# Kernel tuning notes

Hardware: AMD Instinct MI355X
Metric: run time of the kernel (lower is better)

The kernel has to match this reference:

```python
import jax, jax.numpy as jnp
import numpy as np

ALPHA = 0.2  # LeakyReLU negative slope (init arg `alpha`)
N, F_IN, F_OUT = 8192, 512, 256


def setup_inputs() -> dict:
    key = jax.random.key(0)
    k1, k2, k3, k4 = jax.random.split(key, 4)
    x = jax.random.normal(k1, (N, F_IN), dtype=jnp.float32)
    adj = jax.random.randint(k2, (N, N), 0, 2, dtype=jnp.int32)
    W = jax.random.normal(k3, (F_IN, F_OUT), dtype=jnp.float32) * (1.0 / np.sqrt(F_IN))
    a = jax.random.normal(k4, (2 * F_OUT, 1), dtype=jnp.float32) * (1.0 / np.sqrt(F_IN))
    return {"x": x, "adj": adj, "W": W, "a": a}


def reference(x, adj, W, a):
    h = x @ W  # [N, F_OUT]
    f_out = W.shape[1]
    # e[i,j] = LeakyReLU(a1 . h_i + a2 . h_j); computed without the O(N^2*2F) concat
    f1 = h @ a[:f_out, 0]   # [N]
    f2 = h @ a[f_out:, 0]   # [N]
    s = f1[:, None] + f2[None, :]  # [N, N]
    e = jnp.where(s >= 0, s, ALPHA * s)
    # Faithful to the source bug: -9e15 * zeros_like == zeros, so masked entries are 0.0
    att = jnp.where(adj > 0, e, jnp.zeros((), dtype=e.dtype))
    att = jax.nn.softmax(att, axis=1)
    # dropout is identity in eval mode
    h_prime = att @ h  # [N, F_OUT]
    return jax.nn.elu(h_prime)  # concat=True branch
```

## Files before the change

kernel.cpp:

```cpp
#include <hip/hip_runtime.h>
#include <stdint.h>

#define NN 8192
#define FIN 512
#define FOUT 256
#define ALPHA 0.2f
#define KSPLIT 4
#define JT 64
#define NT ((NN / KSPLIT) / JT)

typedef float f32x4 __attribute__((ext_vector_type(4)));
typedef short s16x8 __attribute__((ext_vector_type(8)));

__device__ __forceinline__ uint16_t f2bf(float f) {
  union { float f; uint32_t u; } v; v.f = f;
  uint32_t u = v.u + 0x7fffu + ((v.u >> 16) & 1u);
  return (uint16_t)(u >> 16);
}

__global__ __launch_bounds__(256) void k_wa(const float* __restrict__ W,
                                            const float* __restrict__ a,
                                            float* __restrict__ wa1, float* __restrict__ wa2) {
  __shared__ float a1[256], a2[256];
  int tid = threadIdx.x;
  a1[tid] = a[tid];
  a2[tid] = a[tid + 256];
  __syncthreads();
  int m = blockIdx.x * 256 + tid;
  const float* wrow = W + (size_t)m * FOUT;
  float s1 = 0.f, s2 = 0.f;
  for (int k = 0; k < FOUT; k += 4) {
    f32x4 v = *(const f32x4*)(wrow + k);
#pragma unroll
    for (int i = 0; i < 4; i++) {
      s1 += v[i] * a1[k + i];
      s2 += v[i] * a2[k + i];
    }
  }
  wa1[m] = s1; wa2[m] = s2;
}

__global__ __launch_bounds__(256) void k_f1f2(const float* __restrict__ x,
                                              const float* __restrict__ wa1,
                                              const float* __restrict__ wa2,
                                              float* __restrict__ f1, float* __restrict__ f2,
                                              uint16_t* __restrict__ xb,
                                              float* __restrict__ l_arr) {
  __shared__ float s1[512], s2[512];
  int tid = threadIdx.x;
  if (tid < 4) l_arr[blockIdx.x * 4 + tid] = 0.f;
  s1[tid] = wa1[tid]; s1[tid + 256] = wa1[tid + 256];
  s2[tid] = wa2[tid]; s2[tid + 256] = wa2[tid + 256];
  __syncthreads();
  int w = tid >> 6, l = tid & 63;
  int row = blockIdx.x * 4 + w;
  const float* xr = x + (size_t)row * FIN + l * 8;
  f32x4 v0 = *(const f32x4*)xr;
  f32x4 v1 = *(const f32x4*)(xr + 4);
  uint4 pk;
  pk.x = (uint32_t)f2bf(v0[0]) | ((uint32_t)f2bf(v0[1]) << 16);
  pk.y = (uint32_t)f2bf(v0[2]) | ((uint32_t)f2bf(v0[3]) << 16);
  pk.z = (uint32_t)f2bf(v1[0]) | ((uint32_t)f2bf(v1[1]) << 16);
  pk.w = (uint32_t)f2bf(v1[2]) | ((uint32_t)f2bf(v1[3]) << 16);
  *(uint4*)(xb + (size_t)row * FIN + l * 8) = pk;
  int kb = l * 8;
  float d1 = 0.f, d2 = 0.f;
#pragma unroll
  for (int i = 0; i < 4; i++) {
    d1 += v0[i] * s1[kb + i] + v1[i] * s1[kb + 4 + i];
    d2 += v0[i] * s2[kb + i] + v1[i] * s2[kb + 4 + i];
  }
#pragma unroll
  for (int off = 32; off; off >>= 1) {
    d1 += __shfl_down(d1, off);
    d2 += __shfl_down(d2, off);
  }
  if (l == 0) { f1[row] = d1; f2[row] = d2; }
}

__global__ __launch_bounds__(256) void k_prep_wt(const float* __restrict__ W,
                                                 uint16_t* __restrict__ wt) {
  int idx = blockIdx.x * 256 + threadIdx.x;
  int f  = idx >> 7;
  int k4 = (idx & 127) * 4;
  ushort4 o;
  o.x = f2bf(W[(size_t)(k4 + 0) * FOUT + f]);
  o.y = f2bf(W[(size_t)(k4 + 1) * FOUT + f]);
  o.z = f2bf(W[(size_t)(k4 + 2) * FOUT + f]);
  o.w = f2bf(W[(size_t)(k4 + 3) * FOUT + f]);
  *(ushort4*)(wt + (size_t)f * FIN + k4) = o;
}

__global__ __launch_bounds__(256, 2) void k_gemm_h(const uint16_t* __restrict__ xb,
                                                   const uint16_t* __restrict__ wt,
                                                   uint16_t* __restrict__ h) {
  __shared__ uint16_t Xs[64][40];
  __shared__ uint16_t Ws[64][40];
  int i0 = blockIdx.x * 64;
  int f0 = blockIdx.y * 64;
  int tid = threadIdx.x;
  int w = tid >> 6, l = tid & 63;
  int q = l >> 4, r16 = l & 15;
  f32x4 acc[4];
#pragma unroll
  for (int b = 0; b < 4; b++) acc[b] = (f32x4)0.f;

  int srow = tid >> 2, sch = tid & 3;
  for (int k0 = 0; k0 < FIN; k0 += 32) {
    uint4 xv = *(const uint4*)(xb + (size_t)(i0 + srow) * FIN + k0 + sch * 8);
    uint4 wv = *(const uint4*)(wt + (size_t)(f0 + srow) * FIN + k0 + sch * 8);
    *(uint4*)(&Xs[srow][sch * 8]) = xv;
    *(uint4*)(&Ws[srow][sch * 8]) = wv;
    __syncthreads();
    s16x8 A = *(const s16x8*)(&Xs[w * 16 + r16][q * 8]);
    s16x8 B[4];
#pragma unroll
    for (int b = 0; b < 4; b++) B[b] = *(const s16x8*)(&Ws[b * 16 + r16][q * 8]);
#pragma unroll
    for (int b = 0; b < 4; b++)
      acc[b] = __builtin_amdgcn_mfma_f32_16x16x32_bf16(A, B[b], acc[b], 0, 0, 0);
    __syncthreads();
  }
#pragma unroll
  for (int b = 0; b < 4; b++)
#pragma unroll
    for (int reg = 0; reg < 4; reg++) {
      int row = i0 + w * 16 + q * 4 + reg;
      int col = f0 + b * 16 + r16;
      h[(size_t)row * FOUT + col] = f2bf(acc[b][reg]);
    }
}

__global__ __launch_bounds__(256) void k_transpose(const uint16_t* __restrict__ h,
                                                   uint16_t* __restrict__ ht) {
  __shared__ uint16_t T[64][72];
  int i0 = blockIdx.x * 64, f0 = blockIdx.y * 64;
  int tid = threadIdx.x;
#pragma unroll
  for (int p = 0; p < 2; p++) {
    int idx = tid + p * 256;
    int r = idx >> 3, c8 = idx & 7;
    uint4 v = *(const uint4*)(h + (size_t)(i0 + r) * FOUT + f0 + c8 * 8);
    *(uint4*)(&T[r][c8 * 8]) = v;
  }
  __syncthreads();
#pragma unroll
  for (int p = 0; p < 2; p++) {
    int idx = tid + p * 256;
    int fr = idx >> 3, ic8 = idx & 7;
    s16x8 v;
#pragma unroll
    for (int j = 0; j < 8; j++) v[j] = (short)T[ic8 * 8 + j][fr];
    *(s16x8*)(ht + (size_t)(f0 + fr) * NN + i0 + ic8 * 8) = v;
  }
}

__global__ __launch_bounds__(256, 2) void k_att(const int* __restrict__ adj,
                                                const uint16_t* __restrict__ ht,
                                                const float* __restrict__ f1,
                                                const float* __restrict__ f2,
                                                float* __restrict__ l_arr,
                                                float* __restrict__ part) {
  __shared__ uint16_t Ps[2][64][72];
  __shared__ uint16_t Hs[256][72];
  __shared__ float Fs[NN / KSPLIT];
  int i0 = blockIdx.x * 64;
  int jbase = blockIdx.y * (NN / KSPLIT);
  int tid = threadIdx.x;
  int w = tid >> 6, l = tid & 63;
  int q = l >> 4, r16 = l & 15;
  int prow = tid >> 2, pch = tid & 3;
  int hr8 = l >> 3, hc8 = l & 7;
  float f1i = f1[i0 + prow];
  float lsum = 0.f;

  {
    f32x4 a0 = *(const f32x4*)(f2 + jbase + tid * 8);
    f32x4 a1 = *(const f32x4*)(f2 + jbase + tid * 8 + 4);
    *(f32x4*)(&Fs[tid * 8]) = a0;
    *(f32x4*)(&Fs[tid * 8 + 4]) = a1;
  }
  __syncthreads();

  f32x4 acc[4][4];
#pragma unroll
  for (int a = 0; a < 4; a++)
#pragma unroll
    for (int b = 0; b < 4; b++) acc[a][b] = (f32x4)0.f;

  const int* arow = adj + (size_t)(i0 + prow) * NN + jbase + pch * 16;
  const uint16_t* hrow = ht + (size_t)(w * 64 + hr8) * NN + jbase + hc8 * 8;

  int4 adv[4];
  uint4 hv[8];
#pragma unroll
  for (int t = 0; t < 4; ++t) adv[t] = *(const int4*)(arow + t * 4);
#pragma unroll
  for (int p = 0; p < 8; ++p) hv[p] = *(const uint4*)(hrow + (size_t)p * 8 * NN);

  for (int s = 0; s < NT; ++s) {
    int jl = s * JT;
    f32x4 F0 = *(const f32x4*)(&Fs[jl + pch * 16]);
    f32x4 F1 = *(const f32x4*)(&Fs[jl + pch * 16 + 4]);
    f32x4 F2 = *(const f32x4*)(&Fs[jl + pch * 16 + 8]);
    f32x4 F3 = *(const f32x4*)(&Fs[jl + pch * 16 + 12]);
    s16x8 pv0, pv1;
#define PC(dst, kk, Ac, Fc) { float s_ = f1i + (Fc); float e_ = s_ > 0.f ? s_ : ALPHA * s_; \
      float p_ = ((Ac) != 0) ? __expf(e_) : 1.0f; lsum += p_; dst[kk] = (short)f2bf(p_); }
    PC(pv0, 0, adv[0].x, F0[0]) PC(pv0, 1, adv[0].y, F0[1])
    PC(pv0, 2, adv[0].z, F0[2]) PC(pv0, 3, adv[0].w, F0[3])
    PC(pv0, 4, adv[1].x, F1[0]) PC(pv0, 5, adv[1].y, F1[1])
    PC(pv0, 6, adv[1].z, F1[2]) PC(pv0, 7, adv[1].w, F1[3])
    PC(pv1, 0, adv[2].x, F2[0]) PC(pv1, 1, adv[2].y, F2[1])
    PC(pv1, 2, adv[2].z, F2[2]) PC(pv1, 3, adv[2].w, F2[3])
    PC(pv1, 4, adv[3].x, F3[0]) PC(pv1, 5, adv[3].y, F3[1])
    PC(pv1, 6, adv[3].z, F3[2]) PC(pv1, 7, adv[3].w, F3[3])
#undef PC
    uint16_t (*Pc)[72] = Ps[s & 1];
    *(s16x8*)(&Pc[prow][pch * 16]) = pv0;
    *(s16x8*)(&Pc[prow][pch * 16 + 8]) = pv1;
#pragma unroll
    for (int p = 0; p < 8; ++p)
      *(uint4*)(&Hs[w * 64 + p * 8 + hr8][hc8 * 8]) = hv[p];
    if (s + 1 < NT) {
      int jn = jl + JT;
#pragma unroll
      for (int t = 0; t < 4; ++t) adv[t] = *(const int4*)(arow + jn + t * 4);
#pragma unroll
      for (int p = 0; p < 8; ++p) hv[p] = *(const uint4*)(hrow + (size_t)p * 8 * NN + jn);
    }
    asm volatile("s_waitcnt lgkmcnt(0)" ::: "memory");
    __builtin_amdgcn_s_barrier();
    asm volatile("" ::: "memory");
#pragma unroll
    for (int c = 0; c < 2; ++c) {
      s16x8 Af[4], Bf[4];
#pragma unroll
      for (int a = 0; a < 4; ++a) Af[a] = *(const s16x8*)(&Pc[a * 16 + r16][c * 32 + q * 8]);
#pragma unroll
      for (int b = 0; b < 4; ++b) Bf[b] = *(const s16x8*)(&Hs[w * 64 + b * 16 + r16][c * 32 + q * 8]);
#pragma unroll
      for (int a = 0; a < 4; ++a)
#pragma unroll
        for (int b = 0; b < 4; ++b)
          acc[a][b] = __builtin_amdgcn_mfma_f32_16x16x32_bf16(Af[a], Bf[b], acc[a][b], 0, 0, 0);
    }
  }

  lsum += __shfl_down(lsum, 2);
  lsum += __shfl_down(lsum, 1);
  if (pch == 0) atomicAdd(&l_arr[i0 + prow], lsum);

  float* pb = part + (size_t)blockIdx.y * ((size_t)NN * FOUT);
#pragma unroll
  for (int a = 0; a < 4; a++)
#pragma unroll
    for (int b = 0; b < 4; b++)
#pragma unroll
      for (int reg = 0; reg < 4; reg++) {
        int row = i0 + a * 16 + q * 4 + reg;
        int col = w * 64 + b * 16 + r16;
        pb[(size_t)row * FOUT + col] = acc[a][b][reg];
      }
}

__global__ __launch_bounds__(256) void k_combine(const float* __restrict__ part,
                                                 const float* __restrict__ l_arr,
                                                 float* __restrict__ out) {
  int idx = (blockIdx.x * 256 + threadIdx.x) * 4;
  float r = 1.0f / l_arr[idx >> 8];
  f32x4 sum = (f32x4)0.f;
#pragma unroll
  for (int p = 0; p < KSPLIT; p++)
    sum += *(const f32x4*)(part + (size_t)p * (NN * FOUT) + idx);
  f32x4 o;
#pragma unroll
  for (int i = 0; i < 4; i++) {
    float v = sum[i] * r;
    o[i] = v > 0.f ? v : (__expf(v) - 1.f);
  }
  *(f32x4*)(out + idx) = o;
}

extern "C" void kernel_launch(void* const* d_in, const int* in_sizes, int n_in,
                              void* d_out, int out_size, void* d_ws, size_t ws_size,
                              hipStream_t stream) {
  const float* x   = (const float*)d_in[0];
  const int*   adj = (const int*)d_in[1];
  const float* W   = (const float*)d_in[2];
  const float* a   = (const float*)d_in[3];
  float* out = (float*)d_out;

  char* ws = (char*)d_ws;
  float*    wa1   = (float*)ws;
  float*    wa2   = wa1 + 512;
  float*    f1    = wa2 + 512;
  float*    f2    = f1 + NN;
  float*    l_arr = f2 + NN;
  uint16_t* wt    = (uint16_t*)(l_arr + NN);
  uint16_t* xb    = wt + (size_t)FOUT * FIN;
  uint16_t* h     = xb + (size_t)NN * FIN;
  uint16_t* ht    = h + (size_t)NN * FOUT;
  float*    part  = (float*)(ht + (size_t)NN * FOUT);

  k_wa<<<2, 256, 0, stream>>>(W, a, wa1, wa2);
  k_f1f2<<<NN / 4, 256, 0, stream>>>(x, wa1, wa2, f1, f2, xb, l_arr);
  k_prep_wt<<<128, 256, 0, stream>>>(W, wt);
  k_gemm_h<<<dim3(NN / 64, FOUT / 64), 256, 0, stream>>>(xb, wt, h);
  k_transpose<<<dim3(NN / 64, FOUT / 64), 256, 0, stream>>>(h, ht);
  k_att<<<dim3(NN / 64, KSPLIT), 256, 0, stream>>>(adj, ht, f1, f2, l_arr, part);
  k_combine<<<NN * FOUT / 1024, 256, 0, stream>>>(part, l_arr, out);
}
```

Baseline: 539.4 us.

## Shrink attention tile to 32x32 and raise occupancy in k_att

Restructures the fused attention kernel to use 32-row by 32-column tiles instead of 64x64. It drops the shared-memory f2 staging in favour of direct global loads, shrinks LDS and register use, and raises launch bounds to 4 blocks per CU with twice as many blocks in the grid. The aim is more parallelism and occupancy for the memory-bound adjacency stream. The cost is that the ht tile is reloaded from L2 twice as often per output row and each barrier now covers only one MFMA k-step.

```diff
diff --git a/kernel.cpp b/kernel.cpp
--- a/kernel.cpp
+++ b/kernel.cpp
@@ -6,7 +6,8 @@
 #define FOUT 256
 #define ALPHA 0.2f
 #define KSPLIT 4
-#define JT 64
+#define JT 32
+#define IT 32
 #define NT ((NN / KSPLIT) / JT)
 
 typedef float f32x4 __attribute__((ext_vector_type(4)));
@@ -155,105 +156,87 @@
   }
 }
 
-__global__ __launch_bounds__(256, 2) void k_att(const int* __restrict__ adj,
+__global__ __launch_bounds__(256, 4) void k_att(const int* __restrict__ adj,
                                                 const uint16_t* __restrict__ ht,
                                                 const float* __restrict__ f1,
                                                 const float* __restrict__ f2,
                                                 float* __restrict__ l_arr,
                                                 float* __restrict__ part) {
-  __shared__ uint16_t Ps[2][64][72];
-  __shared__ uint16_t Hs[256][72];
-  __shared__ float Fs[NN / KSPLIT];
-  int i0 = blockIdx.x * 64;
+  __shared__ uint16_t Ps[2][32][40];
+  __shared__ uint16_t Hs[256][40];
+  int i0 = blockIdx.x * IT;
   int jbase = blockIdx.y * (NN / KSPLIT);
   int tid = threadIdx.x;
   int w = tid >> 6, l = tid & 63;
   int q = l >> 4, r16 = l & 15;
-  int prow = tid >> 2, pch = tid & 3;
-  int hr8 = l >> 3, hc8 = l & 7;
+  int prow = tid >> 3, pch = tid & 7;
+  int hr = l >> 2, hc = l & 3;
   float f1i = f1[i0 + prow];
   float lsum = 0.f;
 
-  {
-    f32x4 a0 = *(const f32x4*)(f2 + jbase + tid * 8);
-    f32x4 a1 = *(const f32x4*)(f2 + jbase + tid * 8 + 4);
-    *(f32x4*)(&Fs[tid * 8]) = a0;
-    *(f32x4*)(&Fs[tid * 8 + 4]) = a1;
-  }
-  __syncthreads();
-
-  f32x4 acc[4][4];
-#pragma unroll
-  for (int a = 0; a < 4; a++)
+  const int*      arow = adj + (size_t)(i0 + prow) * NN + jbase + pch * 4;
+  const float*    frow = f2 + jbase + pch * 4;
+  const uint16_t* hrow = ht + (size_t)(w * 64 + hr) * NN + jbase + hc * 8;
+
+  f32x4 acc[2][4];
+#pragma unroll
+  for (int a = 0; a < 2; a++)
 #pragma unroll
     for (int b = 0; b < 4; b++) acc[a][b] = (f32x4)0.f;
 
-  const int* arow = adj + (size_t)(i0 + prow) * NN + jbase + pch * 16;
-  const uint16_t* hrow = ht + (size_t)(w * 64 + hr8) * NN + jbase + hc8 * 8;
-
-  int4 adv[4];
-  uint4 hv[8];
-#pragma unroll
-  for (int t = 0; t < 4; ++t) adv[t] = *(const int4*)(arow + t * 4);
-#pragma unroll
-  for (int p = 0; p < 8; ++p) hv[p] = *(const uint4*)(hrow + (size_t)p * 8 * NN);
+  int4 adv = *(const int4*)(arow);
+  f32x4 F  = *(const f32x4*)(frow);
+  uint4 hv[4];
+#pragma unroll
+  for (int p = 0; p < 4; ++p) hv[p] = *(const uint4*)(hrow + (size_t)p * 16 * NN);
 
   for (int s = 0; s < NT; ++s) {
-    int jl = s * JT;
-    f32x4 F0 = *(const f32x4*)(&Fs[jl + pch * 16]);
-    f32x4 F1 = *(const f32x4*)(&Fs[jl + pch * 16 + 4]);
-    f32x4 F2 = *(const f32x4*)(&Fs[jl + pch * 16 + 8]);
-    f32x4 F3 = *(const f32x4*)(&Fs[jl + pch * 16 + 12]);
-    s16x8 pv0, pv1;
-#define PC(dst, kk, Ac, Fc) { float s_ = f1i + (Fc); float e_ = s_ > 0.f ? s_ : ALPHA * s_; \
-      float p_ = ((Ac) != 0) ? __expf(e_) : 1.0f; lsum += p_; dst[kk] = (short)f2bf(p_); }
-    PC(pv0, 0, adv[0].x, F0[0]) PC(pv0, 1, adv[0].y, F0[1])
-    PC(pv0, 2, adv[0].z, F0[2]) PC(pv0, 3, adv[0].w, F0[3])
-    PC(pv0, 4, adv[1].x, F1[0]) PC(pv0, 5, adv[1].y, F1[1])
-    PC(pv0, 6, adv[1].z, F1[2]) PC(pv0, 7, adv[1].w, F1[3])
-    PC(pv1, 0, adv[2].x, F2[0]) PC(pv1, 1, adv[2].y, F2[1])
-    PC(pv1, 2, adv[2].z, F2[2]) PC(pv1, 3, adv[2].w, F2[3])
-    PC(pv1, 4, adv[3].x, F3[0]) PC(pv1, 5, adv[3].y, F3[1])
-    PC(pv1, 6, adv[3].z, F3[2]) PC(pv1, 7, adv[3].w, F3[3])
+    uint32_t pk0, pk1;
+    {
+      float p0, p1, p2, p3;
+#define PC(dst, Ac, Fc) { float s_ = f1i + (Fc); float e_ = s_ > 0.f ? s_ : ALPHA * s_; \
+        dst = ((Ac) != 0) ? __expf(e_) : 1.0f; lsum += dst; }
+      PC(p0, adv.x, F[0]) PC(p1, adv.y, F[1]) PC(p2, adv.z, F[2]) PC(p3, adv.w, F[3])
 #undef PC
-    uint16_t (*Pc)[72] = Ps[s & 1];
-    *(s16x8*)(&Pc[prow][pch * 16]) = pv0;
-    *(s16x8*)(&Pc[prow][pch * 16 + 8]) = pv1;
-#pragma unroll
-    for (int p = 0; p < 8; ++p)
-      *(uint4*)(&Hs[w * 64 + p * 8 + hr8][hc8 * 8]) = hv[p];
+      pk0 = (uint32_t)f2bf(p0) | ((uint32_t)f2bf(p1) << 16);
+      pk1 = (uint32_t)f2bf(p2) | ((uint32_t)f2bf(p3) << 16);
+    }
+    uint16_t (*Pc)[40] = Ps[s & 1];
+    uint2 pw; pw.x = pk0; pw.y = pk1;
+    *(uint2*)(&Pc[prow][pch * 4]) = pw;
+#pragma unroll
+    for (int p = 0; p < 4; ++p)
+      *(uint4*)(&Hs[w * 64 + p * 16 + hr][hc * 8]) = hv[p];
     if (s + 1 < NT) {
-      int jn = jl + JT;
-#pragma unroll
-      for (int t = 0; t < 4; ++t) adv[t] = *(const int4*)(arow + jn + t * 4);
-#pragma unroll
-      for (int p = 0; p < 8; ++p) hv[p] = *(const uint4*)(hrow + (size_t)p * 8 * NN + jn);
+      int jn = (s + 1) * JT;
+      adv = *(const int4*)(arow + jn);
+      F   = *(const f32x4*)(frow + jn);
+#pragma unroll
+      for (int p = 0; p < 4; ++p) hv[p] = *(const uint4*)(hrow + (size_t)p * 16 * NN + jn);
     }
     asm volatile("s_waitcnt lgkmcnt(0)" ::: "memory");
     __builtin_amdgcn_s_barrier();
     asm volatile("" ::: "memory");
-#pragma unroll
-    for (int c = 0; c < 2; ++c) {
-      s16x8 Af[4], Bf[4];
-#pragma unroll
-      for (int a = 0; a < 4; ++a) Af[a] = *(const s16x8*)(&Pc[a * 16 + r16][c * 32 + q * 8]);
-#pragma unroll
-      for (int b = 0; b < 4; ++b) Bf[b] = *(const s16x8*)(&Hs[w * 64 + b * 16 + r16][c * 32 + q * 8]);
-#pragma unroll
-      for (int a = 0; a < 4; ++a)
-#pragma unroll
-        for (int b = 0; b < 4; ++b)
-          acc[a][b] = __builtin_amdgcn_mfma_f32_16x16x32_bf16(Af[a], Bf[b], acc[a][b], 0, 0, 0);
-    }
-  }
-
+    s16x8 Af[2], Bf[4];
+#pragma unroll
+    for (int a = 0; a < 2; ++a) Af[a] = *(const s16x8*)(&Pc[a * 16 + r16][q * 8]);
+#pragma unroll
+    for (int b = 0; b < 4; ++b) Bf[b] = *(const s16x8*)(&Hs[w * 64 + b * 16 + r16][q * 8]);
+#pragma unroll
+    for (int a = 0; a < 2; ++a)
+#pragma unroll
+      for (int b = 0; b < 4; ++b)
+        acc[a][b] = __builtin_amdgcn_mfma_f32_16x16x32_bf16(Af[a], Bf[b], acc[a][b], 0, 0, 0);
+  }
+
+  lsum += __shfl_down(lsum, 4);
   lsum += __shfl_down(lsum, 2);
   lsum += __shfl_down(lsum, 1);
   if (pch == 0) atomicAdd(&l_arr[i0 + prow], lsum);
 
   float* pb = part + (size_t)blockIdx.y * ((size_t)NN * FOUT);
 #pragma unroll
-  for (int a = 0; a < 4; a++)
+  for (int a = 0; a < 2; a++)
 #pragma unroll
     for (int b = 0; b < 4; b++)
 #pragma unroll
@@ -308,6 +291,6 @@
   k_prep_wt<<<128, 256, 0, stream>>>(W, wt);
   k_gemm_h<<<dim3(NN / 64, FOUT / 64), 256, 0, stream>>>(xb, wt, h);
   k_transpose<<<dim3(NN / 64, FOUT / 64), 256, 0, stream>>>(h, ht);
-  k_att<<<dim3(NN / 64, KSPLIT), 256, 0, stream>>>(adj, ht, f1, f2, l_arr, part);
+  k_att<<<dim3(NN / IT, KSPLIT), 256, 0, stream>>>(adj, ht, f1, f2, l_arr, part);
   k_combine<<<NN * FOUT / 1024, 256, 0, stream>>>(part, l_arr, out);
 }
```

Result: slower. 682.4 us (+26.5%).
